# Optimization experiments

Hardware: AMD Instinct MI355X
Metric: run time of the kernel (lower is better)

Reference implementation:

```python
import jax, jax.numpy as jnp
import numpy as np

DT = 0.042


def setup_inputs() -> dict:
    key = jax.random.key(0)
    ks = jax.random.split(key, 6)
    B, L, I, H = 64, 1024, 128, 512
    x = jax.random.normal(ks[0], (B, L, I), dtype=jnp.float32)
    x2h = jax.random.uniform(ks[1], (I, H), dtype=jnp.float32)  # rand * input_scaling (=1.0)
    h2h = jax.random.normal(ks[2], (H, H), dtype=jnp.float32) * (0.99 / (H ** 0.5))  # spectral-norm scaled
    bias = jax.random.uniform(ks[3], (H,), dtype=jnp.float32) * 2.0 - 1.0
    gamma = jax.random.uniform(ks[4], (H,), dtype=jnp.float32) + 2.0   # in [2, 3)
    epsilon = jax.random.uniform(ks[5], (H,), dtype=jnp.float32) + 4.0  # in [4, 5)
    return {"x": x, "x2h": x2h, "h2h": h2h, "bias": bias, "gamma": gamma, "epsilon": epsilon}


def reference(x, x2h, h2h, bias, gamma, epsilon):
    # x: (B, L, I). Precompute input projection for all timesteps in one GEMM.
    B, L, I = x.shape
    H = h2h.shape[0]
    u = jnp.einsum('bli,ih->blh', x, x2h) + bias  # (B, L, H)

    def step(carry, u_t):
        hy, hz = carry
        hz = hz + DT * (jnp.tanh(u_t + hy @ h2h) - gamma * hy - epsilon * hz)
        hy = hy + DT * hz
        return (hy, hz), hy

    init = (jnp.zeros((B, H), dtype=x.dtype), jnp.zeros((B, H), dtype=x.dtype))
    (hy_final, _), ys = jax.lax.scan(step, init, jnp.swapaxes(u, 0, 1))  # ys: (L, B, H)
    all_states = jnp.swapaxes(ys, 0, 1)  # (B, L, H)
    return all_states, hy_final
```

## Files before the change

kernel.cpp:

```cpp
#include <hip/hip_runtime.h>

#define DT 0.042f
constexpr int B = 64, L = 1024, I = 128, H = 512;

constexpr int NG = 32;
constexpr int NS = 8;
constexpr int GB = B / NG;
constexpr int SC = H / NS;

__global__ __launch_bounds__(256) void k_ugemm(const float* __restrict__ x,
                                               const float* __restrict__ w,
                                               const float* __restrict__ bias,
                                               float* __restrict__ u) {
    __shared__ __align__(16) float a_s[64][132];
    __shared__ __align__(16) float b_s[128][68];
    const int tx = threadIdx.x & 15;
    const int ty = threadIdx.x >> 4;
    const int row0 = blockIdx.x * 64;
    const int col0 = blockIdx.y * 64;

    for (int i = threadIdx.x; i < 64 * 32; i += 256) {
        int r = i >> 5, c4 = (i & 31) << 2;
        *(float4*)&a_s[r][c4] = *(const float4*)(x + (size_t)(row0 + r) * I + c4);
    }
    for (int i = threadIdx.x; i < 128 * 16; i += 256) {
        int k = i >> 4, c4 = (i & 15) << 2;
        *(float4*)&b_s[k][c4] = *(const float4*)(w + (size_t)k * H + col0 + c4);
    }
    __syncthreads();

    float acc[4][4] = {};
    for (int k = 0; k < I; k += 4) {
        float a4[4][4], b4[4][4];
        #pragma unroll
        for (int i = 0; i < 4; ++i) *(float4*)a4[i] = *(const float4*)&a_s[ty * 4 + i][k];
        #pragma unroll
        for (int kk = 0; kk < 4; ++kk) *(float4*)b4[kk] = *(const float4*)&b_s[k + kk][tx * 4];
        #pragma unroll
        for (int i = 0; i < 4; ++i)
            #pragma unroll
            for (int kk = 0; kk < 4; ++kk)
                #pragma unroll
                for (int j = 0; j < 4; ++j)
                    acc[i][j] += a4[i][kk] * b4[kk][j];
    }
    float4 bv = *(const float4*)&bias[col0 + tx * 4];
    #pragma unroll
    for (int i = 0; i < 4; ++i) {
        size_t r = (size_t)(row0 + ty * 4 + i);
        float4 o;
        o.x = acc[i][0] + bv.x; o.y = acc[i][1] + bv.y;
        o.z = acc[i][2] + bv.z; o.w = acc[i][3] + bv.w;
        *(float4*)&u[r * H + col0 + tx * 4] = o;
    }
}

__global__ __launch_bounds__(512, 2) void k_scan(float* __restrict__ su,
                                              const float* __restrict__ h2h,
                                              const float* __restrict__ gamma,
                                              const float* __restrict__ epsv,
                                              unsigned long long* __restrict__ wsq,
                                              float* __restrict__ hyfin) {
    __shared__ __align__(16) float hy_s[GB * H];
    __shared__ __align__(16) float red[2][NS * GB * SC];
    const int tid = threadIdx.x;
    const int g = blockIdx.x & 31;
    const int s = blockIdx.x >> 5;
    const int b0 = g * GB, c0 = s * SC;

    const int cc = tid & 63, kc = tid >> 6;
    const int scc = tid & 63, sb = (tid >> 6) & 1;
    const int sc_ = c0 + scc;

    float hreg[64];
    {
        const float* hp = h2h + (size_t)(kc * 64) * H + c0 + cc;
        #pragma unroll
        for (int kk = 0; kk < 64; ++kk) hreg[kk] = hp[(size_t)kk * H];
    }

    float gam = 0.f, ep = 0.f;
    float* su_p = nullptr;
    if (tid < 128) {
        gam = gamma[sc_]; ep = epsv[sc_];
        su_p = su + (size_t)(b0 + sb) * L * H + sc_;
    }
    unsigned long long* pollA = wsq + (size_t)b0 * H + (size_t)tid * 2;
    unsigned long long* pollB = pollA + (size_t)B * H;
    unsigned long long* dstA  = wsq + (size_t)(b0 + sb) * H + sc_;
    unsigned long long* dstB  = dstA + (size_t)B * H;

    float hy = 0.f, hz = 0.f;
    __syncthreads();

    for (int t = 0; t < L; ++t) {
        float uval = 0.f;
        if (tid < 128) uval = *su_p;

        if (t > 0) {
            unsigned long long* src = (t & 1) ? pollB : pollA;
            const unsigned tg = (unsigned)t;
            ulonglong2 pw;
            asm volatile("global_load_dwordx4 %0, %1, off sc1\n\t"
                         "s_waitcnt vmcnt(0)"
                         : "=v"(pw) : "v"(src) : "memory");
            while ((unsigned)(pw.x >> 32) != tg || (unsigned)(pw.y >> 32) != tg) {
                asm volatile("global_load_dwordx4 %0, %1, off sc1\n\t"
                             "s_waitcnt vmcnt(0)"
                             : "=v"(pw) : "v"(src) : "memory");
            }
            float2 hv;
            hv.x = __uint_as_float((unsigned)pw.x);
            hv.y = __uint_as_float((unsigned)pw.y);
            *(float2*)&hy_s[tid * 2] = hv;
        } else {
            *(float2*)&hy_s[tid * 2] = float2{0.f, 0.f};
        }
        __syncthreads();

        float acc0 = 0.f, acc1 = 0.f;
        const int k0 = kc * 64;
        #pragma unroll
        for (int q = 0; q < 16; ++q) {
            const float4 y0 = *(const float4*)&hy_s[0 * H + k0 + q * 4];
            const float4 y1 = *(const float4*)&hy_s[1 * H + k0 + q * 4];
            acc0 += hreg[q * 4 + 0] * y0.x + hreg[q * 4 + 1] * y0.y
                  + hreg[q * 4 + 2] * y0.z + hreg[q * 4 + 3] * y0.w;
            acc1 += hreg[q * 4 + 0] * y1.x + hreg[q * 4 + 1] * y1.y
                  + hreg[q * 4 + 2] * y1.z + hreg[q * 4 + 3] * y1.w;
        }
        float* rp = red[t & 1];
        rp[kc * (GB * SC) + 0 * SC + cc] = acc0;
        rp[kc * (GB * SC) + 1 * SC + cc] = acc1;
        __syncthreads();

        if (tid < 128) {
            const float* rq = red[t & 1] + sb * SC + scc;
            float m0 = rq[0 * 128] + rq[1 * 128];
            float m1 = rq[2 * 128] + rq[3 * 128];
            float m2 = rq[4 * 128] + rq[5 * 128];
            float m3 = rq[6 * 128] + rq[7 * 128];
            const float xx = uval + ((m0 + m1) + (m2 + m3));
            const float cx = fminf(fmaxf(xx, -10.f), 10.f);
            const float e2 = __expf(2.f * cx);
            const float th = (e2 - 1.f) / (e2 + 1.f);
            hz += DT * (th - gam * hy - ep * hz);
            hy += DT * hz;
            const unsigned long long wq =
                ((unsigned long long)(unsigned)(t + 1) << 32) | __float_as_uint(hy);
            __hip_atomic_store(((t + 1) & 1) ? dstB : dstA, wq,
                               __ATOMIC_RELAXED, __HIP_MEMORY_SCOPE_AGENT);
            *su_p = hy;
            su_p += H;
            if (t == L - 1) hyfin[(size_t)(b0 + sb) * H + sc_] = hy;
        }
    }
}

extern "C" void kernel_launch(void* const* d_in, const int* in_sizes, int n_in,
                              void* d_out, int out_size, void* d_ws, size_t ws_size,
                              hipStream_t stream) {
    const float* x     = (const float*)d_in[0];
    const float* x2h   = (const float*)d_in[1];
    const float* h2h   = (const float*)d_in[2];
    const float* bias  = (const float*)d_in[3];
    const float* gamma = (const float*)d_in[4];
    const float* epsv  = (const float*)d_in[5];
    float* states = (float*)d_out;
    float* hyfin  = states + (size_t)B * L * H;

    unsigned long long* wsq = (unsigned long long*)d_ws;

    hipMemsetAsync(d_ws, 0, 2ull * B * H * 8, stream);
    dim3 g1(B * L / 64, H / 64);
    k_ugemm<<<g1, 256, 0, stream>>>(x, x2h, bias, states);
    k_scan<<<NG * NS, 512, 0, stream>>>(states, h2h, gamma, epsv, wsq, hyfin);
}
```

Measured before the change: 1.885 ms.

## Split scan across one batch row per block, doubling block count

```diff
diff --git a/kernel.cpp b/kernel.cpp
--- a/kernel.cpp
+++ b/kernel.cpp
@@ -3,9 +3,7 @@
 #define DT 0.042f
 constexpr int B = 64, L = 1024, I = 128, H = 512;
 
-constexpr int NG = 32;
 constexpr int NS = 8;
-constexpr int GB = B / NG;
 constexpr int SC = H / NS;
 
 __global__ __launch_bounds__(256) void k_ugemm(const float* __restrict__ x,
@@ -61,33 +59,33 @@
                                               const float* __restrict__ epsv,
                                               unsigned long long* __restrict__ wsq,
                                               float* __restrict__ hyfin) {
-    __shared__ __align__(16) float hy_s[GB * H];
-    __shared__ __align__(16) float red[2][NS * GB * SC];
+    __shared__ __align__(16) float hy_s[H];
+    __shared__ __align__(16) float red[2][H];
     const int tid = threadIdx.x;
-    const int g = blockIdx.x & 31;
-    const int s = blockIdx.x >> 5;
-    const int b0 = g * GB, c0 = s * SC;
+    const int blk = blockIdx.x;
+    const int g = (blk & 31) | ((blk >> 8) << 5);
+    const int s = (blk & 255) >> 5;
+    const int c0 = s * SC;
 
     const int cc = tid & 63, kc = tid >> 6;
-    const int scc = tid & 63, sb = (tid >> 6) & 1;
-    const int sc_ = c0 + scc;
+    const int k0 = kc * 64;
 
     float hreg[64];
     {
-        const float* hp = h2h + (size_t)(kc * 64) * H + c0 + cc;
+        const float* hp = h2h + (size_t)k0 * H + c0 + cc;
         #pragma unroll
         for (int kk = 0; kk < 64; ++kk) hreg[kk] = hp[(size_t)kk * H];
     }
 
     float gam = 0.f, ep = 0.f;
     float* su_p = nullptr;
-    if (tid < 128) {
-        gam = gamma[sc_]; ep = epsv[sc_];
-        su_p = su + (size_t)(b0 + sb) * L * H + sc_;
+    if (tid < SC) {
+        gam = gamma[c0 + tid]; ep = epsv[c0 + tid];
+        su_p = su + (size_t)g * L * H + c0 + tid;
     }
-    unsigned long long* pollA = wsq + (size_t)b0 * H + (size_t)tid * 2;
+    unsigned long long* pollA = wsq + (size_t)g * H + tid;
     unsigned long long* pollB = pollA + (size_t)B * H;
-    unsigned long long* dstA  = wsq + (size_t)(b0 + sb) * H + sc_;
+    unsigned long long* dstA  = wsq + (size_t)g * H + c0 + tid;
     unsigned long long* dstB  = dstA + (size_t)B * H;
 
     float hy = 0.f, hz = 0.f;
@@ -95,51 +93,38 @@
 
     for (int t = 0; t < L; ++t) {
         float uval = 0.f;
-        if (tid < 128) uval = *su_p;
+        if (tid < SC) uval = *su_p;
 
         if (t > 0) {
             unsigned long long* src = (t & 1) ? pollB : pollA;
             const unsigned tg = (unsigned)t;
-            ulonglong2 pw;
-            asm volatile("global_load_dwordx4 %0, %1, off sc1\n\t"
-                         "s_waitcnt vmcnt(0)"
-                         : "=v"(pw) : "v"(src) : "memory");
-            while ((unsigned)(pw.x >> 32) != tg || (unsigned)(pw.y >> 32) != tg) {
-                asm volatile("global_load_dwordx4 %0, %1, off sc1\n\t"
-                             "s_waitcnt vmcnt(0)"
-                             : "=v"(pw) : "v"(src) : "memory");
-            }
-            float2 hv;
-            hv.x = __uint_as_float((unsigned)pw.x);
-            hv.y = __uint_as_float((unsigned)pw.y);
-            *(float2*)&hy_s[tid * 2] = hv;
+            unsigned long long w0 = __hip_atomic_load(src, __ATOMIC_RELAXED,
+                                                      __HIP_MEMORY_SCOPE_AGENT);
+            while ((unsigned)(w0 >> 32) != tg)
+                w0 = __hip_atomic_load(src, __ATOMIC_RELAXED,
+                                       __HIP_MEMORY_SCOPE_AGENT);
+            hy_s[tid] = __uint_as_float((unsigned)w0);
         } else {
-            *(float2*)&hy_s[tid * 2] = float2{0.f, 0.f};
+            hy_s[tid] = 0.f;
         }
         __syncthreads();
 
-        float acc0 = 0.f, acc1 = 0.f;
-        const int k0 = kc * 64;
+        float acc = 0.f;
         #pragma unroll
         for (int q = 0; q < 16; ++q) {
-            const float4 y0 = *(const float4*)&hy_s[0 * H + k0 + q * 4];
-            const float4 y1 = *(const float4*)&hy_s[1 * H + k0 + q * 4];
-            acc0 += hreg[q * 4 + 0] * y0.x + hreg[q * 4 + 1] * y0.y
-                  + hreg[q * 4 + 2] * y0.z + hreg[q * 4 + 3] * y0.w;
-            acc1 += hreg[q * 4 + 0] * y1.x + hreg[q * 4 + 1] * y1.y
-                  + hreg[q * 4 + 2] * y1.z + hreg[q * 4 + 3] * y1.w;
+            const float4 y = *(const float4*)&hy_s[k0 + q * 4];
+            acc += hreg[q * 4 + 0] * y.x + hreg[q * 4 + 1] * y.y
+                 + hreg[q * 4 + 2] * y.z + hreg[q * 4 + 3] * y.w;
         }
-        float* rp = red[t & 1];
-        rp[kc * (GB * SC) + 0 * SC + cc] = acc0;
-        rp[kc * (GB * SC) + 1 * SC + cc] = acc1;
+        red[t & 1][kc * SC + cc] = acc;
         __syncthreads();
 
-        if (tid < 128) {
-            const float* rq = red[t & 1] + sb * SC + scc;
-            float m0 = rq[0 * 128] + rq[1 * 128];
-            float m1 = rq[2 * 128] + rq[3 * 128];
-            float m2 = rq[4 * 128] + rq[5 * 128];
-            float m3 = rq[6 * 128] + rq[7 * 128];
+        if (tid < SC) {
+            const float* rq = red[t & 1] + tid;
+            float m0 = rq[0 * SC] + rq[1 * SC];
+            float m1 = rq[2 * SC] + rq[3 * SC];
+            float m2 = rq[4 * SC] + rq[5 * SC];
+            float m3 = rq[6 * SC] + rq[7 * SC];
             const float xx = uval + ((m0 + m1) + (m2 + m3));
             const float cx = fminf(fmaxf(xx, -10.f), 10.f);
             const float e2 = __expf(2.f * cx);
@@ -152,7 +137,7 @@
                                __ATOMIC_RELAXED, __HIP_MEMORY_SCOPE_AGENT);
             *su_p = hy;
             su_p += H;
-            if (t == L - 1) hyfin[(size_t)(b0 + sb) * H + sc_] = hy;
+            if (t == L - 1) hyfin[(size_t)g * H + c0 + tid] = hy;
         }
     }
 }
@@ -174,5 +159,5 @@
     hipMemsetAsync(d_ws, 0, 2ull * B * H * 8, stream);
     dim3 g1(B * L / 64, H / 64);
     k_ugemm<<<g1, 256, 0, stream>>>(x, x2h, bias, states);
-    k_scan<<<NG * NS, 512, 0, stream>>>(states, h2h, gamma, epsv, wsq, hyfin);
+    k_scan<<<512, 512, 0, stream>>>(states, h2h, gamma, epsv, wsq, hyfin);
 }
```

Measured after the change: 1.862 ms. Within noise of the previous version (-1.2%).
